# Optimization experiments

Hardware: AMD Instinct MI355X
Metric: run time of the kernel (lower is better)

The kernel has to match this reference:

```python
import jax, jax.numpy as jnp
import numpy as np

B, T, D, H, L = 8, 128, 400, 300, 45  # batch, max_length, 2*word_lstm_size, hidden, tag_count


def setup_inputs() -> dict:
    key = jax.random.key(0)
    ks = jax.random.split(key, 10)
    s = 0.05
    return {
        "cont_repr": jax.random.normal(ks[0], (B, T, D), jnp.float32),
        "root": jax.random.normal(ks[1], (1, 1, D), jnp.float32),
        "W1a": jax.random.normal(ks[2], (D, H), jnp.float32) * s,
        "W1b": jax.random.normal(ks[3], (D, H), jnp.float32) * s,
        "b1": jnp.zeros((H,), jnp.float32),
        "Wa": jax.random.normal(ks[4], (H, 1), jnp.float32) * s,
        "ba": jnp.zeros((1,), jnp.float32),
        "Wl": jax.random.normal(ks[5], (H, L), jnp.float32) * s,
        "bl": jnp.zeros((L,), jnp.float32),
        "sentence_lengths": jax.random.randint(ks[6], (B,), 0, T + 1),
        "desired_arcs": jax.random.randint(ks[7], (B, T), 0, T + 1),
        "desired_labels": jax.random.randint(ks[8], (B, T), 0, L),
        "use_desired_arcs": 1,
    }


def reference(cont_repr, root, W1a, W1b, b1, Wa, ba, Wl, bl,
              sentence_lengths, desired_arcs, desired_labels, use_desired_arcs):
    b, t, d = cont_repr.shape
    mask = (jnp.arange(t)[None, :] < sentence_lengths[:, None]).astype(cont_repr.dtype)  # [B,T]
    n_valid = jnp.maximum(mask.sum(), 1.0)

    # Dense(concat(tile_a, tile_b)) == tile_a @ W1a + tile_b @ W1b (exact same math,
    # avoids materializing the [B,T,T+1,2D] concat the TF graph builds).
    a_proj = jnp.einsum('btd,dh->bth', cont_repr, W1a)                     # [B,T,H]
    with_root = jnp.concatenate([jnp.broadcast_to(root, (b, 1, d)), cont_repr], axis=1)  # [B,T+1,D]
    b_proj = jnp.einsum('bsd,dh->bsh', with_root, W1b)                     # [B,T+1,H]
    h = jax.nn.relu(a_proj[:, :, None, :] + b_proj[:, None, :, :] + b1)    # [B,T,T+1,H]

    # UAS: arc scorer (units=1) over T+1 head candidates
    arc_logits = jnp.einsum('btsh,ho->btso', h, Wa)[..., 0] + ba[0]        # [B,T,T+1]
    predicted_arcs = jnp.argmax(arc_logits, axis=-1)                        # [B,T]
    arc_logp = jax.nn.log_softmax(arc_logits, axis=-1)
    arc_ce = -jnp.take_along_axis(arc_logp, desired_arcs[..., None], axis=-1)[..., 0]
    uas_loss = (arc_ce * mask).sum() / n_valid

    # LAS: gather pair repr at selected head, score labels
    sel = desired_arcs if use_desired_arcs else predicted_arcs             # [B,T]
    idx = jnp.broadcast_to(sel[:, :, None, None], (b, t, 1, h.shape[-1]))
    sel_h = jnp.take_along_axis(h, idx, axis=2)[:, :, 0, :]                # [B,T,H]
    lab_logits = jnp.einsum('bth,hl->btl', sel_h, Wl) + bl                 # [B,T,L]
    lab_logp = jax.nn.log_softmax(lab_logits, axis=-1)
    lab_ce = -jnp.take_along_axis(lab_logp, desired_labels[..., None], axis=-1)[..., 0]
    las_loss = (lab_ce * mask).sum() / n_valid

    return (uas_loss + las_loss) / 2
```

## Files before the change

### kernel.cpp

```cpp
#include <hip/hip_runtime.h>
#include <hip/hip_bf16.h>
#include <math.h>

#define BN 8
#define TT 128
#define DD 400
#define HH 300
#define LL 45
#define SS 129
#define ALG_STRIDE 132
#define PADW 308

__global__ __launch_bounds__(640) void proj_kernel(
    const float* __restrict__ cont, const float* __restrict__ root,
    const float* __restrict__ W1a, const float* __restrict__ W1b,
    const float* __restrict__ b1,
    const int* __restrict__ slen,
    float* __restrict__ AP, float* __restrict__ BPX,
    float* __restrict__ accum)
{
    __shared__ float rows_s[9 * DD];
    const int blk = blockIdx.x;
    const int tid = threadIdx.x;

    const bool isA   = (blk < 128);
    const bool isRB  = (blk == 128);
    const int  u     = isA ? blk : blk - 128;
    const int  row0  = u * 8;

    if (isRB && tid == 0) accum[0] = 0.f;
    if (isA && ((row0 & 127) >= slen[row0 >> 7])) return;

    {
        const float* src = cont + (size_t)row0 * DD;
        for (int i = tid; i < 8 * DD; i += 640) rows_s[i] = src[i];
        for (int i = tid; i < DD; i += 640)     rows_s[8 * DD + i] = root[i];
    }
    __syncthreads();

    const int grp = tid / 320;
    const int h   = tid % 320;
    const bool hok = (h < HH);

    float acc[9];
    #pragma unroll
    for (int r = 0; r < 9; ++r) acc[r] = 0.f;

    if (hok) {
        const float* wp = (isA ? W1a : W1b) + (size_t)(grp * 200) * HH + h;
        const float* rs = rows_s;
        const int dbase = grp * 200;
        #pragma unroll
        for (int dc = 0; dc < 200; dc += 4) {
            const float w0 = wp[(size_t)(dc + 0) * HH];
            const float w1 = wp[(size_t)(dc + 1) * HH];
            const float w2 = wp[(size_t)(dc + 2) * HH];
            const float w3 = wp[(size_t)(dc + 3) * HH];
            #pragma unroll
            for (int r = 0; r < 9; ++r) {
                const float4 ra = *(const float4*)&rs[r * DD + dbase + dc];
                acc[r] = fmaf(ra.x, w0, acc[r]);
                acc[r] = fmaf(ra.y, w1, acc[r]);
                acc[r] = fmaf(ra.z, w2, acc[r]);
                acc[r] = fmaf(ra.w, w3, acc[r]);
            }
        }
    }

    __syncthreads();
    float* red = rows_s;
    if (grp == 1 && hok) {
        #pragma unroll
        for (int r = 0; r < 9; ++r) red[h * 9 + r] = acc[r];
    }
    __syncthreads();
    if (grp == 0 && hok) {
        float tot[9];
        #pragma unroll
        for (int r = 0; r < 9; ++r) tot[r] = acc[r] + red[h * 9 + r];
        if (isA) {
            const float bb = b1[h];
            float* dst = AP + (size_t)row0 * HH + h;
            #pragma unroll
            for (int r = 0; r < 8; ++r) dst[(size_t)r * HH] = tot[r] + bb;
        } else {
            const int b = row0 >> 7, t = row0 & 127;
            float* dst = BPX + ((size_t)(b * SS + t + 1)) * HH + h;
            #pragma unroll
            for (int r = 0; r < 8; ++r) dst[(size_t)r * HH] = tot[r];
            if (isRB) {
                #pragma unroll
                for (int bb2 = 0; bb2 < BN; ++bb2)
                    BPX[(size_t)bb2 * SS * HH + h] = tot[8];
            }
        }
    }
}

__global__ __launch_bounds__(256) void arc_kernel(
    const float* __restrict__ AP, const float* __restrict__ BPX,
    const float* __restrict__ Wa, const int* __restrict__ slen,
    float* __restrict__ ALG)
{
    __shared__ float ap_s[8][PADW];
    __shared__ float bp_s[33][PADW];
    __shared__ float wa_s[PADW];

    const int blk = blockIdx.x;
    const int b  = blk >> 6;
    const int tt = (blk >> 2) & 15;
    const int sc = blk & 3;
    const int t0 = tt * 8;
    if (t0 >= slen[b]) return;

    const int tid  = threadIdx.x;
    const int lane = tid & 63;
    const int wave = tid >> 6;
    const int tl   = lane & 7;
    const int sl   = lane >> 3;
    const int s0   = sc * 32;

    {
        const float* apg = AP + (size_t)(b * TT + t0) * HH;
        for (int i = tid; i < 8 * HH; i += 256)
            ap_s[i / HH][i % HH] = apg[i];
        const float* bpg = BPX + (size_t)(b * SS + s0) * HH;
        for (int i = tid; i < 33 * HH; i += 256)
            bp_s[i / HH][i % HH] = bpg[i];
        for (int i = tid; i < HH; i += 256)
            wa_s[i] = Wa[i];
    }
    __syncthreads();

    const int s_local = wave * 8 + sl;
    const float* aprow = ap_s[tl];
    const float* bprow = bp_s[s_local];

    float acc = 0.f;
    #pragma unroll 5
    for (int hh = 0; hh < HH; hh += 4) {
        const float4 a4 = *(const float4*)&aprow[hh];
        const float4 p4 = *(const float4*)&bprow[hh];
        const float4 w4 = *(const float4*)&wa_s[hh];
        acc = fmaf(fmaxf(a4.x + p4.x, 0.f), w4.x, acc);
        acc = fmaf(fmaxf(a4.y + p4.y, 0.f), w4.y, acc);
        acc = fmaf(fmaxf(a4.z + p4.z, 0.f), w4.z, acc);
        acc = fmaf(fmaxf(a4.w + p4.w, 0.f), w4.w, acc);
    }
    ALG[(size_t)(b * TT + t0 + tl) * ALG_STRIDE + s0 + s_local] = acc;

    if (sc == 3 && wave == 0 && sl == 0) {
        const float* bpr = bp_s[32];
        float a2 = 0.f;
        #pragma unroll 5
        for (int hh = 0; hh < HH; hh += 4) {
            const float4 a4 = *(const float4*)&aprow[hh];
            const float4 p4 = *(const float4*)&bpr[hh];
            const float4 w4 = *(const float4*)&wa_s[hh];
            a2 = fmaf(fmaxf(a4.x + p4.x, 0.f), w4.x, a2);
            a2 = fmaf(fmaxf(a4.y + p4.y, 0.f), w4.y, a2);
            a2 = fmaf(fmaxf(a4.z + p4.z, 0.f), w4.z, a2);
            a2 = fmaf(fmaxf(a4.w + p4.w, 0.f), w4.w, a2);
        }
        ALG[(size_t)(b * TT + t0 + tl) * ALG_STRIDE + 128] = a2;
    }
}

__global__ __launch_bounds__(256) void smx_kernel(
    const float* __restrict__ AP, const float* __restrict__ BPX,
    const float* __restrict__ Wl, const float* __restrict__ bl,
    const float* __restrict__ ALG,
    const int* __restrict__ slen, const int* __restrict__ des_arcs,
    const int* __restrict__ des_labels, const int* __restrict__ use_des,
    float* __restrict__ accum)
{
    const int blk = blockIdx.x;
    const int b = blk >> 7, t = blk & 127;
    if (t >= slen[b]) return;
    const int tid  = threadIdx.x;
    const int lane = tid & 63;
    const int wave = tid >> 6;

    __shared__ float selh[HH];
    __shared__ float partial[4][64];
    __shared__ float arc_ce_s;
    __shared__ int   sel_s;

    if (wave == 0) {
        const float* lg = ALG + (size_t)blk * ALG_STRIDE;
        const float v0 = lg[lane];
        const float v1 = lg[64 + lane];
        const float v2 = (lane == 0) ? lg[128] : -INFINITY;

        float m = fmaxf(fmaxf(v0, v1), v2);
        #pragma unroll
        for (int off = 32; off; off >>= 1) m = fmaxf(m, __shfl_xor(m, off, 64));
        float e = __expf(v0 - m) + __expf(v1 - m) + ((lane == 0) ? __expf(v2 - m) : 0.f);
        #pragma unroll
        for (int off = 32; off; off >>= 1) e += __shfl_xor(e, off, 64);
        const float arc_lse = m + __logf(e);

        float bv = v0; int bi = lane;
        if (v1 > bv) { bv = v1; bi = 64 + lane; }
        if (lane == 0 && v2 > bv) { bv = v2; bi = 128; }
        #pragma unroll
        for (int off = 32; off; off >>= 1) {
            const float ov = __shfl_xor(bv, off, 64);
            const int   oi = __shfl_xor(bi, off, 64);
            if (ov > bv || (ov == bv && oi < bi)) { bv = ov; bi = oi; }
        }
        if (lane == 0) {
            const int da = des_arcs[b * TT + t];
            arc_ce_s = arc_lse - lg[da];
            sel_s = use_des[0] ? da : bi;
        }
    }
    __syncthreads();

    {
        const int sel = sel_s;
        const float* ap = AP + (size_t)blk * HH;
        const float* bp = BPX + (size_t)(b * SS + sel) * HH;
        for (int hh = tid; hh < HH; hh += 256)
            selh[hh] = fmaxf(ap[hh] + bp[hh], 0.f);
    }
    __syncthreads();

    {
        float p = 0.f;
        if (lane < LL) {
            const int h0 = wave * 75;
            #pragma unroll 5
            for (int j = 0; j < 75; ++j)
                p = fmaf(selh[h0 + j], Wl[(h0 + j) * LL + lane], p);
        }
        partial[wave][lane] = p;
    }
    __syncthreads();

    if (wave == 0) {
        float a = -INFINITY;
        if (lane < LL)
            a = bl[lane] + partial[0][lane] + partial[1][lane]
                         + partial[2][lane] + partial[3][lane];
        float lm = a;
        #pragma unroll
        for (int off = 32; off; off >>= 1) lm = fmaxf(lm, __shfl_xor(lm, off, 64));
        float le = (lane < LL) ? __expf(a - lm) : 0.f;
        #pragma unroll
        for (int off = 32; off; off >>= 1) le += __shfl_xor(le, off, 64);
        const float lab_lse = lm + __logf(le);

        const int dl = des_labels[b * TT + t];
        const float ldl = __shfl(a, dl, 64);
        if (lane == 0)
            atomicAdd(accum, arc_ce_s + (lab_lse - ldl));
    }
}

__global__ void finalize_kernel(const float* __restrict__ accum,
                                const int* __restrict__ slen,
                                float* __restrict__ out)
{
    if (threadIdx.x == 0) {
        int n = 0;
        for (int b = 0; b < BN; ++b) {
            int l = slen[b];
            if (l < 0) l = 0;
            if (l > TT) l = TT;
            n += l;
        }
        float nv = (float)n;
        if (nv < 1.f) nv = 1.f;
        out[0] = accum[0] / (2.f * nv);
    }
}

extern "C" void kernel_launch(void* const* d_in, const int* in_sizes, int n_in,
                              void* d_out, int out_size, void* d_ws, size_t ws_size,
                              hipStream_t stream) {
    const float* cont = (const float*)d_in[0];
    const float* root = (const float*)d_in[1];
    const float* W1a  = (const float*)d_in[2];
    const float* W1b  = (const float*)d_in[3];
    const float* b1   = (const float*)d_in[4];
    const float* Wa   = (const float*)d_in[5];
    const float* Wl   = (const float*)d_in[7];
    const float* bl   = (const float*)d_in[8];
    const int* slen   = (const int*)d_in[9];
    const int* darc   = (const int*)d_in[10];
    const int* dlab   = (const int*)d_in[11];
    const int* used   = (const int*)d_in[12];
    float* out = (float*)d_out;

    float* AP    = (float*)d_ws;
    float* BPX   = AP  + 1024 * HH;
    float* ALG   = BPX + BN * SS * HH;
    float* accum = ALG + 1024 * ALG_STRIDE;

    proj_kernel<<<256, 640, 0, stream>>>(cont, root, W1a, W1b, b1, slen, AP, BPX, accum);
    arc_kernel<<<512, 256, 0, stream>>>(AP, BPX, Wa, slen, ALG);
    smx_kernel<<<1024, 256, 0, stream>>>(AP, BPX, Wl, bl, ALG, slen, darc, dlab, used, accum);
    finalize_kernel<<<1, 64, 0, stream>>>(accum, slen, out);
}
```

Before: 53.99 us.

## Fuse arc scoring, softmax/label scoring and finalize into one kernel

Merges the arc-logit kernel, the per-token softmax/label kernel and the finalize kernel into a single kernel. Each block handles 4 tokens, streams all 129 head rows through shared memory in chunks of 16, and keeps the logits in shared memory instead of a global ALG buffer. A last-block ticket counter writes the final output. This removes two launches and the global logit round trip, but each block now streams the whole BPX row set, so far fewer blocks (256 versus 512) do more serial chunked work with extra barriers.

```diff
diff --git a/kernel.cpp b/kernel.cpp
--- a/kernel.cpp
+++ b/kernel.cpp
@@ -8,8 +8,6 @@
 #define HH 300
 #define LL 45
 #define SS 129
-#define ALG_STRIDE 132
-#define PADW 308
 
 __global__ __launch_bounds__(640) void proj_kernel(
     const float* __restrict__ cont, const float* __restrict__ root,
@@ -17,7 +15,7 @@
     const float* __restrict__ b1,
     const int* __restrict__ slen,
     float* __restrict__ AP, float* __restrict__ BPX,
-    float* __restrict__ accum)
+    float* __restrict__ accum, int* __restrict__ ticket)
 {
     __shared__ float rows_s[9 * DD];
     const int blk = blockIdx.x;
@@ -28,7 +26,7 @@
     const int  u     = isA ? blk : blk - 128;
     const int  row0  = u * 8;
 
-    if (isRB && tid == 0) accum[0] = 0.f;
+    if (isRB && tid == 0) { accum[0] = 0.f; ticket[0] = 0; }
     if (isA && ((row0 & 127) >= slen[row0 >> 7])) return;
 
     {
@@ -97,182 +95,148 @@
     }
 }
 
-__global__ __launch_bounds__(256) void arc_kernel(
+__global__ __launch_bounds__(256) void arcsmx_kernel(
     const float* __restrict__ AP, const float* __restrict__ BPX,
-    const float* __restrict__ Wa, const int* __restrict__ slen,
-    float* __restrict__ ALG)
+    const float* __restrict__ Wa, const float* __restrict__ Wl,
+    const float* __restrict__ bl,
+    const int* __restrict__ slen, const int* __restrict__ darc,
+    const int* __restrict__ dlab, const int* __restrict__ used,
+    float* __restrict__ accum, int* __restrict__ ticket,
+    float* __restrict__ out)
 {
-    __shared__ float ap_s[8][PADW];
-    __shared__ float bp_s[33][PADW];
-    __shared__ float wa_s[PADW];
+    __shared__ float ap_s[4][HH];
+    __shared__ float wa_s[HH];
+    __shared__ float bp_s[16][HH];
+    __shared__ float lg_s[4][132];
+    __shared__ float part_s[64][5];
+    __shared__ float selh[4][HH];
 
     const int blk = blockIdx.x;
-    const int b  = blk >> 6;
-    const int tt = (blk >> 2) & 15;
-    const int sc = blk & 3;
-    const int t0 = tt * 8;
-    if (t0 >= slen[b]) return;
-
+    const int b  = blk >> 5;
+    const int tg = blk & 31;
+    const int t0 = tg * 4;
     const int tid  = threadIdx.x;
     const int lane = tid & 63;
-    const int wave = tid >> 6;
-    const int tl   = lane & 7;
-    const int sl   = lane >> 3;
-    const int s0   = sc * 32;
-
-    {
-        const float* apg = AP + (size_t)(b * TT + t0) * HH;
-        for (int i = tid; i < 8 * HH; i += 256)
-            ap_s[i / HH][i % HH] = apg[i];
-        const float* bpg = BPX + (size_t)(b * SS + s0) * HH;
-        for (int i = tid; i < 33 * HH; i += 256)
-            bp_s[i / HH][i % HH] = bpg[i];
-        for (int i = tid; i < HH; i += 256)
-            wa_s[i] = Wa[i];
-    }
-    __syncthreads();
-
-    const int s_local = wave * 8 + sl;
-    const float* aprow = ap_s[tl];
-    const float* bprow = bp_s[s_local];
-
-    float acc = 0.f;
-    #pragma unroll 5
-    for (int hh = 0; hh < HH; hh += 4) {
-        const float4 a4 = *(const float4*)&aprow[hh];
-        const float4 p4 = *(const float4*)&bprow[hh];
-        const float4 w4 = *(const float4*)&wa_s[hh];
-        acc = fmaf(fmaxf(a4.x + p4.x, 0.f), w4.x, acc);
-        acc = fmaf(fmaxf(a4.y + p4.y, 0.f), w4.y, acc);
-        acc = fmaf(fmaxf(a4.z + p4.z, 0.f), w4.z, acc);
-        acc = fmaf(fmaxf(a4.w + p4.w, 0.f), w4.w, acc);
-    }
-    ALG[(size_t)(b * TT + t0 + tl) * ALG_STRIDE + s0 + s_local] = acc;
-
-    if (sc == 3 && wave == 0 && sl == 0) {
-        const float* bpr = bp_s[32];
-        float a2 = 0.f;
-        #pragma unroll 5
-        for (int hh = 0; hh < HH; hh += 4) {
-            const float4 a4 = *(const float4*)&aprow[hh];
-            const float4 p4 = *(const float4*)&bpr[hh];
-            const float4 w4 = *(const float4*)&wa_s[hh];
-            a2 = fmaf(fmaxf(a4.x + p4.x, 0.f), w4.x, a2);
-            a2 = fmaf(fmaxf(a4.y + p4.y, 0.f), w4.y, a2);
-            a2 = fmaf(fmaxf(a4.z + p4.z, 0.f), w4.z, a2);
-            a2 = fmaf(fmaxf(a4.w + p4.w, 0.f), w4.w, a2);
-        }
-        ALG[(size_t)(b * TT + t0 + tl) * ALG_STRIDE + 128] = a2;
-    }
-}
-
-__global__ __launch_bounds__(256) void smx_kernel(
-    const float* __restrict__ AP, const float* __restrict__ BPX,
-    const float* __restrict__ Wl, const float* __restrict__ bl,
-    const float* __restrict__ ALG,
-    const int* __restrict__ slen, const int* __restrict__ des_arcs,
-    const int* __restrict__ des_labels, const int* __restrict__ use_des,
-    float* __restrict__ accum)
-{
-    const int blk = blockIdx.x;
-    const int b = blk >> 7, t = blk & 127;
-    if (t >= slen[b]) return;
-    const int tid  = threadIdx.x;
-    const int lane = tid & 63;
-    const int wave = tid >> 6;
-
-    __shared__ float selh[HH];
-    __shared__ float partial[4][64];
-    __shared__ float arc_ce_s;
-    __shared__ int   sel_s;
-
-    if (wave == 0) {
-        const float* lg = ALG + (size_t)blk * ALG_STRIDE;
-        const float v0 = lg[lane];
-        const float v1 = lg[64 + lane];
-        const float v2 = (lane == 0) ? lg[128] : -INFINITY;
-
-        float m = fmaxf(fmaxf(v0, v1), v2);
-        #pragma unroll
-        for (int off = 32; off; off >>= 1) m = fmaxf(m, __shfl_xor(m, off, 64));
-        float e = __expf(v0 - m) + __expf(v1 - m) + ((lane == 0) ? __expf(v2 - m) : 0.f);
-        #pragma unroll
-        for (int off = 32; off; off >>= 1) e += __shfl_xor(e, off, 64);
-        const float arc_lse = m + __logf(e);
-
-        float bv = v0; int bi = lane;
-        if (v1 > bv) { bv = v1; bi = 64 + lane; }
-        if (lane == 0 && v2 > bv) { bv = v2; bi = 128; }
-        #pragma unroll
-        for (int off = 32; off; off >>= 1) {
-            const float ov = __shfl_xor(bv, off, 64);
-            const int   oi = __shfl_xor(bi, off, 64);
-            if (ov > bv || (ov == bv && oi < bi)) { bv = ov; bi = oi; }
-        }
-        if (lane == 0) {
-            const int da = des_arcs[b * TT + t];
-            arc_ce_s = arc_lse - lg[da];
-            sel_s = use_des[0] ? da : bi;
-        }
-    }
-    __syncthreads();
-
-    {
-        const int sel = sel_s;
-        const float* ap = AP + (size_t)blk * HH;
-        const float* bp = BPX + (size_t)(b * SS + sel) * HH;
-        for (int hh = tid; hh < HH; hh += 256)
-            selh[hh] = fmaxf(ap[hh] + bp[hh], 0.f);
-    }
-    __syncthreads();
-
-    {
-        float p = 0.f;
-        if (lane < LL) {
-            const int h0 = wave * 75;
-            #pragma unroll 5
-            for (int j = 0; j < 75; ++j)
-                p = fmaf(selh[h0 + j], Wl[(h0 + j) * LL + lane], p);
-        }
-        partial[wave][lane] = p;
-    }
-    __syncthreads();
-
-    if (wave == 0) {
-        float a = -INFINITY;
-        if (lane < LL)
-            a = bl[lane] + partial[0][lane] + partial[1][lane]
-                         + partial[2][lane] + partial[3][lane];
-        float lm = a;
-        #pragma unroll
-        for (int off = 32; off; off >>= 1) lm = fmaxf(lm, __shfl_xor(lm, off, 64));
-        float le = (lane < LL) ? __expf(a - lm) : 0.f;
-        #pragma unroll
-        for (int off = 32; off; off >>= 1) le += __shfl_xor(le, off, 64);
-        const float lab_lse = lm + __logf(le);
-
-        const int dl = des_labels[b * TT + t];
-        const float ldl = __shfl(a, dl, 64);
-        if (lane == 0)
-            atomicAdd(accum, arc_ce_s + (lab_lse - ldl));
-    }
-}
-
-__global__ void finalize_kernel(const float* __restrict__ accum,
-                                const int* __restrict__ slen,
-                                float* __restrict__ out)
-{
-    if (threadIdx.x == 0) {
-        int n = 0;
-        for (int b = 0; b < BN; ++b) {
-            int l = slen[b];
-            if (l < 0) l = 0;
-            if (l > TT) l = TT;
-            n += l;
-        }
-        float nv = (float)n;
-        if (nv < 1.f) nv = 1.f;
-        out[0] = accum[0] / (2.f * nv);
+    const int wv   = tid >> 6;
+    const int len  = slen[b];
+
+    if (t0 < len) {
+        {
+            const float* apg = AP + (size_t)(b * TT + t0) * HH;
+            for (int i = tid; i < 4 * HH; i += 256) ap_s[i / HH][i % HH] = apg[i];
+            for (int i = tid; i < HH; i += 256)     wa_s[i] = Wa[i];
+        }
+        __syncthreads();
+
+        const int tl = tid & 3;
+        const int sl = (tid >> 2) & 15;
+        const int qq = tid >> 6;
+        const int h0 = qq * 76;
+        const int hn = (qq == 3) ? 72 : 76;
+
+        for (int c = 0; c < 9; ++c) {
+            const int s0 = c * 16;
+            const int nrows = (c == 8) ? 1 : 16;
+            const float* bpg = BPX + ((size_t)b * SS + s0) * HH;
+            for (int i = tid; i < nrows * HH; i += 256)
+                bp_s[i / HH][i % HH] = bpg[i];
+            __syncthreads();
+
+            float p = 0.f;
+            if (sl < nrows) {
+                const float* ar = ap_s[tl];
+                const float* br = bp_s[sl];
+                for (int hh = h0; hh < h0 + hn; hh += 4) {
+                    const float4 a4 = *(const float4*)&ar[hh];
+                    const float4 b4 = *(const float4*)&br[hh];
+                    const float4 w4 = *(const float4*)&wa_s[hh];
+                    p = fmaf(fmaxf(a4.x + b4.x, 0.f), w4.x, p);
+                    p = fmaf(fmaxf(a4.y + b4.y, 0.f), w4.y, p);
+                    p = fmaf(fmaxf(a4.z + b4.z, 0.f), w4.z, p);
+                    p = fmaf(fmaxf(a4.w + b4.w, 0.f), w4.w, p);
+                }
+            }
+            part_s[tid & 63][qq] = p;
+            __syncthreads();
+            if (qq == 0 && sl < nrows) {
+                const int pid = tid & 63;
+                lg_s[tl][s0 + sl] = part_s[pid][0] + part_s[pid][1]
+                                  + part_s[pid][2] + part_s[pid][3];
+            }
+            __syncthreads();
+        }
+
+        const int t = t0 + wv;
+        if (t < len) {
+            const float* lg = lg_s[wv];
+            const float v0 = lg[lane];
+            const float v1 = lg[64 + lane];
+            const float v2 = (lane == 0) ? lg[128] : -INFINITY;
+
+            float m = fmaxf(fmaxf(v0, v1), v2);
+            #pragma unroll
+            for (int off = 32; off; off >>= 1) m = fmaxf(m, __shfl_xor(m, off, 64));
+            float e = __expf(v0 - m) + __expf(v1 - m) + ((lane == 0) ? __expf(v2 - m) : 0.f);
+            #pragma unroll
+            for (int off = 32; off; off >>= 1) e += __shfl_xor(e, off, 64);
+            const float arc_lse = m + __logf(e);
+
+            float bv = v0; int bi = lane;
+            if (v1 > bv) { bv = v1; bi = 64 + lane; }
+            if (lane == 0 && v2 > bv) { bv = v2; bi = 128; }
+            #pragma unroll
+            for (int off = 32; off; off >>= 1) {
+                const float ov = __shfl_xor(bv, off, 64);
+                const int   oi = __shfl_xor(bi, off, 64);
+                if (ov > bv || (ov == bv && oi < bi)) { bv = ov; bi = oi; }
+            }
+            const int da = darc[b * TT + t];
+            const float arc_ce = arc_lse - lg[da];
+            const int sel = used[0] ? da : bi;
+
+            const float* bp = BPX + ((size_t)b * SS + sel) * HH;
+            for (int hh = lane; hh < HH; hh += 64)
+                selh[wv][hh] = fmaxf(ap_s[wv][hh] + bp[hh], 0.f);
+
+            float a0 = 0.f, a1 = 0.f;
+            if (lane < LL) {
+                a0 = bl[lane];
+                for (int hh = 0; hh < HH; hh += 4) {
+                    a0 = fmaf(selh[wv][hh + 0], Wl[(hh + 0) * LL + lane], a0);
+                    a1 = fmaf(selh[wv][hh + 1], Wl[(hh + 1) * LL + lane], a1);
+                    a0 = fmaf(selh[wv][hh + 2], Wl[(hh + 2) * LL + lane], a0);
+                    a1 = fmaf(selh[wv][hh + 3], Wl[(hh + 3) * LL + lane], a1);
+                }
+            }
+            const float a = (lane < LL) ? (a0 + a1) : -INFINITY;
+            float lm = a;
+            #pragma unroll
+            for (int off = 32; off; off >>= 1) lm = fmaxf(lm, __shfl_xor(lm, off, 64));
+            float le = (lane < LL) ? __expf(a - lm) : 0.f;
+            #pragma unroll
+            for (int off = 32; off; off >>= 1) le += __shfl_xor(le, off, 64);
+            const float lab_lse = lm + __logf(le);
+
+            const int dl = dlab[b * TT + t];
+            const float adl = __shfl(a, dl, 64);
+            if (lane == 0)
+                atomicAdd(accum, arc_ce + (lab_lse - adl));
+        }
+    }
+
+    __syncthreads();
+    if (tid == 0) {
+        __threadfence();
+        if (atomicAdd(ticket, 1) == 255) {
+            int n = 0;
+            #pragma unroll
+            for (int bb = 0; bb < BN; ++bb) {
+                int l = slen[bb]; l = l < 0 ? 0 : (l > TT ? TT : l); n += l;
+            }
+            float nv = (float)n; if (nv < 1.f) nv = 1.f;
+            const float total = atomicAdd(accum, 0.f);
+            out[0] = total / (2.f * nv);
+        }
     }
 }
 
@@ -293,13 +257,13 @@
     const int* used   = (const int*)d_in[12];
     float* out = (float*)d_out;
 
-    float* AP    = (float*)d_ws;
-    float* BPX   = AP  + 1024 * HH;
-    float* ALG   = BPX + BN * SS * HH;
-    float* accum = ALG + 1024 * ALG_STRIDE;
-
-    proj_kernel<<<256, 640, 0, stream>>>(cont, root, W1a, W1b, b1, slen, AP, BPX, accum);
-    arc_kernel<<<512, 256, 0, stream>>>(AP, BPX, Wa, slen, ALG);
-    smx_kernel<<<1024, 256, 0, stream>>>(AP, BPX, Wl, bl, ALG, slen, darc, dlab, used, accum);
-    finalize_kernel<<<1, 64, 0, stream>>>(accum, slen, out);
+    float* AP     = (float*)d_ws;
+    float* BPX    = AP + 1024 * HH;
+    float* accum  = BPX + BN * SS * HH;
+    int*   ticket = (int*)(accum + 16);
+
+    proj_kernel<<<256, 640, 0, stream>>>(cont, root, W1a, W1b, b1, slen,
+                                         AP, BPX, accum, ticket);
+    arcsmx_kernel<<<256, 256, 0, stream>>>(AP, BPX, Wa, Wl, bl, slen,
+                                           darc, dlab, used, accum, ticket, out);
 }
```

Measured after the change: 67.43 us. +24.9%, slower.
